# Kernel optimization log

Measured on AMD Instinct MI355X. Metric: run time of the kernel, lower is better.

## Reference

```python
import jax, jax.numpy as jnp
import numpy as np

T = 8192   # sequence length (= max_seq_len)
E = 1024   # embedding dim
D = 11     # hard-coded projection dim in source


def setup_inputs() -> dict:
    key = jax.random.key(0)
    ks = jax.random.split(key, 6)
    s_e = 1.0 / np.sqrt(E)
    s_d = 1.0 / np.sqrt(D)
    return {
        "x": jax.random.randint(ks[0], (T,), 0, 32000, dtype=jnp.int64),
        "x_embeddings": jax.random.normal(ks[1], (T, E), dtype=jnp.float32),
        "Wk": jax.random.normal(ks[2], (D, E), dtype=jnp.float32) * s_e,
        "bk": jnp.zeros((D,), dtype=jnp.float32),
        "Wq": jax.random.normal(ks[3], (D, E), dtype=jnp.float32) * s_e,
        "bq": jnp.zeros((D,), dtype=jnp.float32),
        "Wv": jax.random.normal(ks[4], (D, E), dtype=jnp.float32) * s_e,
        "bv": jnp.zeros((D,), dtype=jnp.float32),
        "Wf": jax.random.normal(ks[5], (E, D), dtype=jnp.float32) * s_d,
        "bf": jnp.zeros((E,), dtype=jnp.float32),
    }


def reference(x, x_embeddings, Wk, bk, Wq, bq, Wv, bv, Wf, bf):
    t = x.shape[0]  # static under jit
    k = x_embeddings @ Wk.T + bk            # [T, D]
    q = x_embeddings @ Wq.T + bq            # [T, D]
    v = x_embeddings @ Wv.T + bv            # [T, D]
    att = q @ k.T                           # [T, T]; NOTE: no 1/sqrt(D) scaling in source
    causal = jnp.tril(jnp.ones((t, t), dtype=bool))
    att = jnp.where(causal, att, -jnp.inf)
    att = jax.nn.softmax(att, axis=1)       # dim=1 as in source
    res = att @ v                           # [T, D]
    return res @ Wf.T + bf                  # [T, E]
```

## Files before the change

### kernel.cpp

```cpp
#include <hip/hip_runtime.h>

#define T_SEQ 8192
#define E_DIM 1024
#define QS 36
#define QNEC 16
#define QKC 64
#define QX4 16
#define QXST 17
#define QRB 64
#define AJC 64
#define ARB 128
#define KVW 24
#define TR 16
#define LOG2E 1.4426950408889634f

__device__ __forceinline__ float2 pkfma(float2 a, float2 b, float2 c) {
    return make_float2(fmaf(a.x, b.x, c.x), fmaf(a.y, b.y, c.y));
}
__device__ __forceinline__ float2 f2(float x, float y) { return make_float2(x, y); }


__global__ __launch_bounds__(256) void prep_wf(const float* __restrict__ Wf,
                                               float* __restrict__ Wfp) {
    int id = blockIdx.x * 256 + threadIdx.x;
    if (id >= E_DIM * 12) return;
    int e = id / 12, d = id % 12;
    Wfp[id] = (d < 11) ? Wf[(size_t)e * 11 + d] : 0.f;
}

__global__ __launch_bounds__(256) void qkv_proj(
    const float* __restrict__ xe,
    const float* __restrict__ Wk, const float* __restrict__ bk,
    const float* __restrict__ Wq, const float* __restrict__ bq,
    const float* __restrict__ Wv, const float* __restrict__ bv,
    float* __restrict__ partQ) {
    const int row0 = blockIdx.x * QRB;
    const int ec = blockIdx.y;
    const int lane = threadIdx.x & 63;
    const int wg = threadIdx.x >> 6;
    const int cb = ec * QKC;

    __shared__ float4 xT[QRB * QXST];
    __shared__ float4 wT[36 * QX4];

#pragma unroll
    for (int t = 0; t < 4; ++t) {
        int idx = threadIdx.x + t * 256;
        int r = idx >> 4, c4 = idx & 15;
        xT[r * QXST + c4] =
            *(const float4*)(xe + (size_t)(row0 + r) * E_DIM + cb + c4 * 4);
    }
    for (int idx = threadIdx.x; idx < 36 * QX4; idx += 256) {
        int r = idx >> 4, c4 = idx & 15;
        float4 v = make_float4(0.f, 0.f, 0.f, 0.f);
        if (r < 33) {
            const float* base = (r < 11) ? (Wk + (size_t)r * E_DIM)
                              : (r < 22) ? (Wq + (size_t)(r - 11) * E_DIM)
                                         : (Wv + (size_t)(r - 22) * E_DIM);
            v = *(const float4*)(base + cb + c4 * 4);
        }
        wT[idx] = v;
    }
    __syncthreads();

    float2 acc[9];
#pragma unroll
    for (int k = 0; k < 9; ++k) acc[k] = f2(0.f, 0.f);

    const float4* xr = xT + lane * QXST;
    const float4* wr = wT + wg * 9 * QX4;
#pragma unroll 4
    for (int c4 = 0; c4 < QX4; ++c4) {
        float4 xv = xr[c4];
#pragma unroll
        for (int k = 0; k < 9; ++k) {
            float4 wv = wr[k * QX4 + c4];
            acc[k] = pkfma(f2(xv.x, xv.y), f2(wv.x, wv.y), acc[k]);
            acc[k] = pkfma(f2(xv.z, xv.w), f2(wv.z, wv.w), acc[k]);
        }
    }

    __syncthreads();
    float* res = (float*)xT;
#pragma unroll
    for (int k = 0; k < 9; ++k) {
        int o = wg * 9 + k;
        bool live = (o < 33);
        int c = (o < 11) ? o : (o < 22) ? o + 1 : (o < 33) ? o + 2
              : (o == 33) ? 11 : (o == 34) ? 23 : 35;
        float b = 0.f;
        if (ec == 0 && live)
            b = (o < 11) ? bk[o] : (o < 22) ? bq[o - 11] : bv[o - 22];
        res[lane * 36 + c] = live ? (acc[k].x + acc[k].y + b) : 0.f;
    }
    __syncthreads();

    float4* dst = (float4*)(partQ + ((size_t)ec * T_SEQ + row0) * QS);
    for (int idx = threadIdx.x; idx < QRB * 9; idx += 256) {
        int r = idx / 9, f = idx % 9;
        dst[idx] = *(const float4*)(res + r * 36 + f * 4);
    }
}

__global__ __launch_bounds__(256) void reduceQ(const float* __restrict__ partQ,
                                               float* __restrict__ qkvF) {
    const size_t idx = (size_t)blockIdx.x * 256 + threadIdx.x;
    const float4* p = (const float4*)partQ;
    const size_t cs = (size_t)T_SEQ * (QS / 4);
    float4 s = make_float4(0.f, 0.f, 0.f, 0.f);
#pragma unroll
    for (int c = 0; c < QNEC; ++c) {
        float4 a = p[idx + (size_t)c * cs];
        s.x += a.x; s.y += a.y; s.z += a.z; s.w += a.w;
    }
    ((float4*)qkvF)[idx] = s;
}

__global__ __launch_bounds__(64) void attn(const float* __restrict__ qkvF,
                                           float* __restrict__ part) {
    const int b = blockIdx.x;
    int rb = 0;
    while ((rb + 1) * (rb + 2) / 2 <= b) ++rb;
    const int s = b - rb * (rb + 1) / 2;
    const int lane = threadIdx.x;
    const int r0 = rb * ARB + lane * 2;

    const float* qp0 = qkvF + (size_t)r0 * QS + 12;
    const float* qp1 = qp0 + QS;
    float2 qa[6], qb[6];
#pragma unroll
    for (int d = 0; d < 5; ++d) {
        qa[d] = f2(qp0[2 * d], qp0[2 * d + 1]);
        qb[d] = f2(qp1[2 * d], qp1[2 * d + 1]);
    }
    qa[5] = f2(qp0[10], 0.f);
    qb[5] = f2(qp1[10], 0.f);

    float2 oa[6], ob[6];
#pragma unroll
    for (int d = 0; d < 6; ++d) { oa[d] = f2(0.f, 0.f); ob[d] = f2(0.f, 0.f); }

    __shared__ float kv[AJC * KVW];

#pragma unroll
    for (int pass = 0; pass < 2; ++pass) {
        const int jc = pass ? (2 * rb + 1 - s) : s;
        const int j0 = jc * AJC;
        if (pass) __syncthreads();
#pragma unroll
        for (int t = 0; t < 6; ++t) {
            int idx = lane + t * 64;
            int row = idx / 6, f = idx % 6;
            int srcOff = f * 4 + (f >= 3 ? 12 : 0);
            float4 v = *(const float4*)(qkvF + (size_t)(j0 + row) * QS + srcOff);
            *(float4*)(kv + row * KVW + f * 4) = v;
        }
        __syncthreads();

        for (int jj = 0; jj < AJC; ++jj) {
            const float* kp = kv + jj * KVW;
            const float4 kA = *(const float4*)(kp);
            const float4 kB = *(const float4*)(kp + 4);
            const float4 kC = *(const float4*)(kp + 8);
            const float4 vA = *(const float4*)(kp + 12);
            const float4 vB = *(const float4*)(kp + 16);
            const float4 vC = *(const float4*)(kp + 20);
            const float2 k01 = f2(kA.x, kA.y), k23 = f2(kA.z, kA.w);
            const float2 k45 = f2(kB.x, kB.y), k67 = f2(kB.z, kB.w);
            const float2 k89 = f2(kC.x, kC.y), kXp = f2(kC.z, kC.w);

            float2 sa = pkfma(qa[0], k01, pkfma(qa[1], k23, pkfma(qa[2], k45,
                        pkfma(qa[3], k67, pkfma(qa[4], k89,
                        pkfma(qa[5], kXp, f2(0.f, 0.f)))))));
            float2 sb = pkfma(qb[0], k01, pkfma(qb[1], k23, pkfma(qb[2], k45,
                        pkfma(qb[3], k67, pkfma(qb[4], k89,
                        pkfma(qb[5], kXp, f2(0.f, 0.f)))))));
            float pa = __expf(sa.x + sa.y);
            float pb = __expf(sb.x + sb.y);
            const int j = j0 + jj;
            pa = (j <= r0)     ? pa : 0.f;
            pb = (j <= r0 + 1) ? pb : 0.f;
            float2 pa2 = f2(pa, pa), pb2 = f2(pb, pb);
            oa[0] = pkfma(pa2, f2(vA.x, vA.y), oa[0]);
            oa[1] = pkfma(pa2, f2(vA.z, vA.w), oa[1]);
            oa[2] = pkfma(pa2, f2(vB.x, vB.y), oa[2]);
            oa[3] = pkfma(pa2, f2(vB.z, vB.w), oa[3]);
            oa[4] = pkfma(pa2, f2(vC.x, vC.y), oa[4]);
            oa[5] = pkfma(pa2, f2(vC.z, 1.f),  oa[5]);
            ob[0] = pkfma(pb2, f2(vA.x, vA.y), ob[0]);
            ob[1] = pkfma(pb2, f2(vA.z, vA.w), ob[1]);
            ob[2] = pkfma(pb2, f2(vB.x, vB.y), ob[2]);
            ob[3] = pkfma(pb2, f2(vB.z, vB.w), ob[3]);
            ob[4] = pkfma(pb2, f2(vC.x, vC.y), ob[4]);
            ob[5] = pkfma(pb2, f2(vC.z, 1.f),  ob[5]);
        }
    }

    float* d0 = part + ((size_t)s * T_SEQ + r0) * 12;
    float4 t;
    t.x = oa[0].x; t.y = oa[0].y; t.z = oa[1].x; t.w = oa[1].y; *(float4*)(d0 + 0) = t;
    t.x = oa[2].x; t.y = oa[2].y; t.z = oa[3].x; t.w = oa[3].y; *(float4*)(d0 + 4) = t;
    t.x = oa[4].x; t.y = oa[4].y; t.z = oa[5].x; t.w = oa[5].y; *(float4*)(d0 + 8) = t;
    float* d1 = d0 + 12;
    t.x = ob[0].x; t.y = ob[0].y; t.z = ob[1].x; t.w = ob[1].y; *(float4*)(d1 + 0) = t;
    t.x = ob[2].x; t.y = ob[2].y; t.z = ob[3].x; t.w = ob[3].y; *(float4*)(d1 + 4) = t;
    t.x = ob[4].x; t.y = ob[4].y; t.z = ob[5].x; t.w = ob[5].y; *(float4*)(d1 + 8) = t;
}

__global__ __launch_bounds__(256) void pass2(const float* __restrict__ part,
                                             const float* __restrict__ Wfp,
                                             const float* __restrict__ bf,
                                             float* __restrict__ out) {
    const int t0 = blockIdx.x * TR;
    __shared__ float res[TR][12];
    const int cnt = t0 / ARB + 1;
    if (threadIdx.x < TR * 12) {
        const float* p = part + (size_t)t0 * 12 + threadIdx.x;
        const size_t S = (size_t)T_SEQ * 12;
        float v[4];
#pragma unroll
        for (int u = 0; u < 4; ++u) v[u] = 0.f;
        int c = 0;
        for (; c + 4 <= cnt; c += 4) {
#pragma unroll
            for (int u = 0; u < 4; ++u) v[u] += p[(size_t)(c + u) * S];
        }
        for (; c < cnt; ++c) v[0] += p[(size_t)c * S];
        float sum = (v[0] + v[1]) + (v[2] + v[3]);
        const int d = threadIdx.x % 12;
        res[threadIdx.x / 12][d] = (d == 11) ? (1.f / sum) : sum;
    }
    __syncthreads();

    const int e0 = threadIdx.x * 4;
    float4 wf[4][3];
#pragma unroll
    for (int ee = 0; ee < 4; ++ee) {
        const float4* wp = (const float4*)(Wfp + (size_t)(e0 + ee) * 12);
        wf[ee][0] = wp[0]; wf[ee][1] = wp[1]; wf[ee][2] = wp[2];
    }
    const float4 bv = *(const float4*)(bf + e0);

    for (int r = 0; r < TR; ++r) {
        float rr[12];
#pragma unroll
        for (int d = 0; d < 12; ++d) rr[d] = res[r][d];
        float2 a0 = f2(0.f, 0.f), a1 = a0, a2 = a0, a3 = a0;
#pragma unroll
        for (int d = 0; d < 10; d += 2) {
            float2 rv = f2(rr[d], rr[d + 1]);
            a0 = pkfma(rv, f2(((const float*)&wf[0][0])[d], ((const float*)&wf[0][0])[d + 1]), a0);
            a1 = pkfma(rv, f2(((const float*)&wf[1][0])[d], ((const float*)&wf[1][0])[d + 1]), a1);
            a2 = pkfma(rv, f2(((const float*)&wf[2][0])[d], ((const float*)&wf[2][0])[d + 1]), a2);
            a3 = pkfma(rv, f2(((const float*)&wf[3][0])[d], ((const float*)&wf[3][0])[d + 1]), a3);
        }
        const float rl = rr[11];
        float4 ov;
        ov.x = (a0.x + a0.y + rr[10] * wf[0][2].z) * rl + bv.x;
        ov.y = (a1.x + a1.y + rr[10] * wf[1][2].z) * rl + bv.y;
        ov.z = (a2.x + a2.y + rr[10] * wf[2][2].z) * rl + bv.z;
        ov.w = (a3.x + a3.y + rr[10] * wf[3][2].z) * rl + bv.w;
        *(float4*)(out + (size_t)(t0 + r) * E_DIM + e0) = ov;
    }
}

extern "C" void kernel_launch(void* const* d_in, const int* in_sizes, int n_in,
                              void* d_out, int out_size, void* d_ws, size_t ws_size,
                              hipStream_t stream) {
    const float* xe = (const float*)d_in[1];
    const float* Wk = (const float*)d_in[2];
    const float* bk = (const float*)d_in[3];
    const float* Wq = (const float*)d_in[4];
    const float* bq = (const float*)d_in[5];
    const float* Wv = (const float*)d_in[6];
    const float* bv = (const float*)d_in[7];
    const float* Wf = (const float*)d_in[8];
    const float* bf = (const float*)d_in[9];
    float* out = (float*)d_out;

    float* qkvF  = (float*)d_ws;
    float* wfp   = qkvF + (size_t)T_SEQ * QS;
    float* partQ = wfp + (size_t)E_DIM * 12;
    float* part  = partQ;

    prep_wf<<<(E_DIM * 12 + 255) / 256, 256, 0, stream>>>(Wf, wfp);
    qkv_proj<<<dim3(T_SEQ / QRB, QNEC), 256, 0, stream>>>(xe, Wk, bk, Wq, bq, Wv, bv, partQ);
    reduceQ<<<(T_SEQ * (QS / 4)) / 256, 256, 0, stream>>>(partQ, qkvF);
    const int nrb = T_SEQ / ARB;
    attn<<<nrb * (nrb + 1) / 2, 64, 0, stream>>>(qkvF, part);
    pass2<<<T_SEQ / TR, 256, 0, stream>>>(part, wfp, bf, out);
}
```

Before: 177.8 us.

## Split attention into single-chunk blocks and reduce partials with atomics

Each attention block now handles a single 64-key chunk instead of two paired chunks, which doubles the grid. Partial outputs are accumulated straight into one zero-initialised buffer with float atomicAdd, so the strided multi-partial reduction in pass2 goes away. The zeroing is folded into the existing prep kernel. This trades a longer reduction read and an extra partial buffer for atomic contention (up to 128 adds per element) and non-deterministic summation order.

```diff
diff --git a/kernel.cpp b/kernel.cpp
--- a/kernel.cpp
+++ b/kernel.cpp
@@ -12,7 +12,6 @@
 #define ARB 128
 #define KVW 24
 #define TR 16
-#define LOG2E 1.4426950408889634f
 
 __device__ __forceinline__ float2 pkfma(float2 a, float2 b, float2 c) {
     return make_float2(fmaf(a.x, b.x, c.x), fmaf(a.y, b.y, c.y));
@@ -20,12 +19,17 @@
 __device__ __forceinline__ float2 f2(float x, float y) { return make_float2(x, y); }
 
 
-__global__ __launch_bounds__(256) void prep_wf(const float* __restrict__ Wf,
-                                               float* __restrict__ Wfp) {
+__global__ __launch_bounds__(256) void prep(const float* __restrict__ Wf,
+                                            float* __restrict__ Wfp,
+                                            float* __restrict__ part1) {
     int id = blockIdx.x * 256 + threadIdx.x;
-    if (id >= E_DIM * 12) return;
-    int e = id / 12, d = id % 12;
-    Wfp[id] = (d < 11) ? Wf[(size_t)e * 11 + d] : 0.f;
+    if (id < E_DIM * 12) {
+        int e = id / 12, d = id % 12;
+        Wfp[id] = (d < 11) ? Wf[(size_t)e * 11 + d] : 0.f;
+    } else {
+        int j = id - E_DIM * 12;
+        if (j < T_SEQ * 12) part1[j] = 0.f;
+    }
 }
 
 __global__ __launch_bounds__(256) void qkv_proj(
@@ -117,13 +121,14 @@
 }
 
 __global__ __launch_bounds__(64) void attn(const float* __restrict__ qkvF,
-                                           float* __restrict__ part) {
+                                           float* __restrict__ part1) {
     const int b = blockIdx.x;
     int rb = 0;
-    while ((rb + 1) * (rb + 2) / 2 <= b) ++rb;
-    const int s = b - rb * (rb + 1) / 2;
+    while ((rb + 1) * (rb + 2) <= b) ++rb;
+    const int jc = b - rb * (rb + 1);
     const int lane = threadIdx.x;
     const int r0 = rb * ARB + lane * 2;
+    const int j0 = jc * AJC;
 
     const float* qp0 = qkvF + (size_t)r0 * QS + 12;
     const float* qp1 = qp0 + QS;
@@ -143,92 +148,79 @@
     __shared__ float kv[AJC * KVW];
 
 #pragma unroll
-    for (int pass = 0; pass < 2; ++pass) {
-        const int jc = pass ? (2 * rb + 1 - s) : s;
-        const int j0 = jc * AJC;
-        if (pass) __syncthreads();
-#pragma unroll
-        for (int t = 0; t < 6; ++t) {
-            int idx = lane + t * 64;
-            int row = idx / 6, f = idx % 6;
-            int srcOff = f * 4 + (f >= 3 ? 12 : 0);
-            float4 v = *(const float4*)(qkvF + (size_t)(j0 + row) * QS + srcOff);
-            *(float4*)(kv + row * KVW + f * 4) = v;
-        }
-        __syncthreads();
-
-        for (int jj = 0; jj < AJC; ++jj) {
-            const float* kp = kv + jj * KVW;
-            const float4 kA = *(const float4*)(kp);
-            const float4 kB = *(const float4*)(kp + 4);
-            const float4 kC = *(const float4*)(kp + 8);
-            const float4 vA = *(const float4*)(kp + 12);
-            const float4 vB = *(const float4*)(kp + 16);
-            const float4 vC = *(const float4*)(kp + 20);
-            const float2 k01 = f2(kA.x, kA.y), k23 = f2(kA.z, kA.w);
-            const float2 k45 = f2(kB.x, kB.y), k67 = f2(kB.z, kB.w);
-            const float2 k89 = f2(kC.x, kC.y), kXp = f2(kC.z, kC.w);
-
-            float2 sa = pkfma(qa[0], k01, pkfma(qa[1], k23, pkfma(qa[2], k45,
-                        pkfma(qa[3], k67, pkfma(qa[4], k89,
-                        pkfma(qa[5], kXp, f2(0.f, 0.f)))))));
-            float2 sb = pkfma(qb[0], k01, pkfma(qb[1], k23, pkfma(qb[2], k45,
-                        pkfma(qb[3], k67, pkfma(qb[4], k89,
-                        pkfma(qb[5], kXp, f2(0.f, 0.f)))))));
-            float pa = __expf(sa.x + sa.y);
-            float pb = __expf(sb.x + sb.y);
-            const int j = j0 + jj;
-            pa = (j <= r0)     ? pa : 0.f;
-            pb = (j <= r0 + 1) ? pb : 0.f;
-            float2 pa2 = f2(pa, pa), pb2 = f2(pb, pb);
-            oa[0] = pkfma(pa2, f2(vA.x, vA.y), oa[0]);
-            oa[1] = pkfma(pa2, f2(vA.z, vA.w), oa[1]);
-            oa[2] = pkfma(pa2, f2(vB.x, vB.y), oa[2]);
-            oa[3] = pkfma(pa2, f2(vB.z, vB.w), oa[3]);
-            oa[4] = pkfma(pa2, f2(vC.x, vC.y), oa[4]);
-            oa[5] = pkfma(pa2, f2(vC.z, 1.f),  oa[5]);
-            ob[0] = pkfma(pb2, f2(vA.x, vA.y), ob[0]);
-            ob[1] = pkfma(pb2, f2(vA.z, vA.w), ob[1]);
-            ob[2] = pkfma(pb2, f2(vB.x, vB.y), ob[2]);
-            ob[3] = pkfma(pb2, f2(vB.z, vB.w), ob[3]);
-            ob[4] = pkfma(pb2, f2(vC.x, vC.y), ob[4]);
-            ob[5] = pkfma(pb2, f2(vC.z, 1.f),  ob[5]);
-        }
-    }
-
-    float* d0 = part + ((size_t)s * T_SEQ + r0) * 12;
-    float4 t;
-    t.x = oa[0].x; t.y = oa[0].y; t.z = oa[1].x; t.w = oa[1].y; *(float4*)(d0 + 0) = t;
-    t.x = oa[2].x; t.y = oa[2].y; t.z = oa[3].x; t.w = oa[3].y; *(float4*)(d0 + 4) = t;
-    t.x = oa[4].x; t.y = oa[4].y; t.z = oa[5].x; t.w = oa[5].y; *(float4*)(d0 + 8) = t;
+    for (int t = 0; t < 6; ++t) {
+        int idx = lane + t * 64;
+        int row = idx / 6, f = idx % 6;
+        int srcOff = f * 4 + (f >= 3 ? 12 : 0);
+        float4 v = *(const float4*)(qkvF + (size_t)(j0 + row) * QS + srcOff);
+        *(float4*)(kv + row * KVW + f * 4) = v;
+    }
+    __syncthreads();
+
+    for (int jj = 0; jj < AJC; ++jj) {
+        const float* kp = kv + jj * KVW;
+        const float4 kA = *(const float4*)(kp);
+        const float4 kB = *(const float4*)(kp + 4);
+        const float4 kC = *(const float4*)(kp + 8);
+        const float4 vA = *(const float4*)(kp + 12);
+        const float4 vB = *(const float4*)(kp + 16);
+        const float4 vC = *(const float4*)(kp + 20);
+        const float2 k01 = f2(kA.x, kA.y), k23 = f2(kA.z, kA.w);
+        const float2 k45 = f2(kB.x, kB.y), k67 = f2(kB.z, kB.w);
+        const float2 k89 = f2(kC.x, kC.y), kXp = f2(kC.z, kC.w);
+
+        float2 sa = pkfma(qa[0], k01, pkfma(qa[1], k23, pkfma(qa[2], k45,
+                    pkfma(qa[3], k67, pkfma(qa[4], k89,
+                    pkfma(qa[5], kXp, f2(0.f, 0.f)))))));
+        float2 sb = pkfma(qb[0], k01, pkfma(qb[1], k23, pkfma(qb[2], k45,
+                    pkfma(qb[3], k67, pkfma(qb[4], k89,
+                    pkfma(qb[5], kXp, f2(0.f, 0.f)))))));
+        float pa = __expf(sa.x + sa.y);
+        float pb = __expf(sb.x + sb.y);
+        const int j = j0 + jj;
+        pa = (j <= r0)     ? pa : 0.f;
+        pb = (j <= r0 + 1) ? pb : 0.f;
+        float2 pa2 = f2(pa, pa), pb2 = f2(pb, pb);
+        oa[0] = pkfma(pa2, f2(vA.x, vA.y), oa[0]);
+        oa[1] = pkfma(pa2, f2(vA.z, vA.w), oa[1]);
+        oa[2] = pkfma(pa2, f2(vB.x, vB.y), oa[2]);
+        oa[3] = pkfma(pa2, f2(vB.z, vB.w), oa[3]);
+        oa[4] = pkfma(pa2, f2(vC.x, vC.y), oa[4]);
+        oa[5] = pkfma(pa2, f2(vC.z, 1.f),  oa[5]);
+        ob[0] = pkfma(pb2, f2(vA.x, vA.y), ob[0]);
+        ob[1] = pkfma(pb2, f2(vA.z, vA.w), ob[1]);
+        ob[2] = pkfma(pb2, f2(vB.x, vB.y), ob[2]);
+        ob[3] = pkfma(pb2, f2(vB.z, vB.w), ob[3]);
+        ob[4] = pkfma(pb2, f2(vC.x, vC.y), ob[4]);
+        ob[5] = pkfma(pb2, f2(vC.z, 1.f),  ob[5]);
+    }
+
+    float* d0 = part1 + (size_t)r0 * 12;
+    atomicAdd(d0 + 0,  oa[0].x); atomicAdd(d0 + 1,  oa[0].y);
+    atomicAdd(d0 + 2,  oa[1].x); atomicAdd(d0 + 3,  oa[1].y);
+    atomicAdd(d0 + 4,  oa[2].x); atomicAdd(d0 + 5,  oa[2].y);
+    atomicAdd(d0 + 6,  oa[3].x); atomicAdd(d0 + 7,  oa[3].y);
+    atomicAdd(d0 + 8,  oa[4].x); atomicAdd(d0 + 9,  oa[4].y);
+    atomicAdd(d0 + 10, oa[5].x); atomicAdd(d0 + 11, oa[5].y);
     float* d1 = d0 + 12;
-    t.x = ob[0].x; t.y = ob[0].y; t.z = ob[1].x; t.w = ob[1].y; *(float4*)(d1 + 0) = t;
-    t.x = ob[2].x; t.y = ob[2].y; t.z = ob[3].x; t.w = ob[3].y; *(float4*)(d1 + 4) = t;
-    t.x = ob[4].x; t.y = ob[4].y; t.z = ob[5].x; t.w = ob[5].y; *(float4*)(d1 + 8) = t;
-}
-
-__global__ __launch_bounds__(256) void pass2(const float* __restrict__ part,
+    atomicAdd(d1 + 0,  ob[0].x); atomicAdd(d1 + 1,  ob[0].y);
+    atomicAdd(d1 + 2,  ob[1].x); atomicAdd(d1 + 3,  ob[1].y);
+    atomicAdd(d1 + 4,  ob[2].x); atomicAdd(d1 + 5,  ob[2].y);
+    atomicAdd(d1 + 6,  ob[3].x); atomicAdd(d1 + 7,  ob[3].y);
+    atomicAdd(d1 + 8,  ob[4].x); atomicAdd(d1 + 9,  ob[4].y);
+    atomicAdd(d1 + 10, ob[5].x); atomicAdd(d1 + 11, ob[5].y);
+}
+
+__global__ __launch_bounds__(256) void pass2(const float* __restrict__ part1,
                                              const float* __restrict__ Wfp,
                                              const float* __restrict__ bf,
                                              float* __restrict__ out) {
     const int t0 = blockIdx.x * TR;
     __shared__ float res[TR][12];
-    const int cnt = t0 / ARB + 1;
     if (threadIdx.x < TR * 12) {
-        const float* p = part + (size_t)t0 * 12 + threadIdx.x;
-        const size_t S = (size_t)T_SEQ * 12;
-        float v[4];
-#pragma unroll
-        for (int u = 0; u < 4; ++u) v[u] = 0.f;
-        int c = 0;
-        for (; c + 4 <= cnt; c += 4) {
-#pragma unroll
-            for (int u = 0; u < 4; ++u) v[u] += p[(size_t)(c + u) * S];
-        }
-        for (; c < cnt; ++c) v[0] += p[(size_t)c * S];
-        float sum = (v[0] + v[1]) + (v[2] + v[3]);
+        float v = part1[(size_t)t0 * 12 + threadIdx.x];
         const int d = threadIdx.x % 12;
-        res[threadIdx.x / 12][d] = (d == 11) ? (1.f / sum) : sum;
+        res[threadIdx.x / 12][d] = (d == 11) ? (1.f / v) : v;
     }
     __syncthreads();
 
@@ -281,12 +273,12 @@
     float* qkvF  = (float*)d_ws;
     float* wfp   = qkvF + (size_t)T_SEQ * QS;
     float* partQ = wfp + (size_t)E_DIM * 12;
-    float* part  = partQ;
-
-    prep_wf<<<(E_DIM * 12 + 255) / 256, 256, 0, stream>>>(Wf, wfp);
+    float* part1 = partQ + (size_t)QNEC * T_SEQ * QS;
+
+    prep<<<(E_DIM * 12 + T_SEQ * 12 + 255) / 256, 256, 0, stream>>>(Wf, wfp, part1);
     qkv_proj<<<dim3(T_SEQ / QRB, QNEC), 256, 0, stream>>>(xe, Wk, bk, Wq, bq, Wv, bv, partQ);
     reduceQ<<<(T_SEQ * (QS / 4)) / 256, 256, 0, stream>>>(partQ, qkvF);
     const int nrb = T_SEQ / ARB;
-    attn<<<nrb * (nrb + 1) / 2, 64, 0, stream>>>(qkvF, part);
-    pass2<<<T_SEQ / TR, 256, 0, stream>>>(part, wfp, bf, out);
-}
+    attn<<<nrb * (nrb + 1), 64, 0, stream>>>(qkvF, part1);
+    pass2<<<T_SEQ / TR, 256, 0, stream>>>(part1, wfp, bf, out);
+}
```

Measured after the change: 531.2 us. +198.7%, slower.

## Split attention key chunks across two waves and drop Wf prep kernel

Applied to the files above, without the earlier changes.

The attention kernel now runs 128 threads per block, and each wave handles one of two adjacent 64-key chunks in parallel instead of one wave looping over two paired chunks. Partials are indexed by key chunk, so pass2 sums twice as many partial slices (2*rb+2). The separate Wf padding kernel is removed and pass2 reads the unpadded Wf directly with scalar loads. This trades one kernel launch and serial per-wave work for more partial-sum traffic in pass2 and a different causal load balance, since the earlier pairing of chunks s and 2rb+1-s gave every block equal work.

```diff
diff --git a/kernel.cpp b/kernel.cpp
--- a/kernel.cpp
+++ b/kernel.cpp
@@ -11,22 +11,14 @@
 #define AJC 64
 #define ARB 128
 #define KVW 24
+#define NSLOT 128
 #define TR 16
-#define LOG2E 1.4426950408889634f
 
 __device__ __forceinline__ float2 pkfma(float2 a, float2 b, float2 c) {
     return make_float2(fmaf(a.x, b.x, c.x), fmaf(a.y, b.y, c.y));
 }
 __device__ __forceinline__ float2 f2(float x, float y) { return make_float2(x, y); }
 
-
-__global__ __launch_bounds__(256) void prep_wf(const float* __restrict__ Wf,
-                                               float* __restrict__ Wfp) {
-    int id = blockIdx.x * 256 + threadIdx.x;
-    if (id >= E_DIM * 12) return;
-    int e = id / 12, d = id % 12;
-    Wfp[id] = (d < 11) ? Wf[(size_t)e * 11 + d] : 0.f;
-}
 
 __global__ __launch_bounds__(256) void qkv_proj(
     const float* __restrict__ xe,
@@ -116,14 +108,17 @@
     ((float4*)qkvF)[idx] = s;
 }
 
-__global__ __launch_bounds__(64) void attn(const float* __restrict__ qkvF,
-                                           float* __restrict__ part) {
+__global__ __launch_bounds__(128) void attn(const float* __restrict__ qkvF,
+                                            float* __restrict__ part) {
     const int b = blockIdx.x;
     int rb = 0;
     while ((rb + 1) * (rb + 2) / 2 <= b) ++rb;
-    const int s = b - rb * (rb + 1) / 2;
-    const int lane = threadIdx.x;
+    const int p = b - rb * (rb + 1) / 2;
+    const int lane = threadIdx.x & 63;
+    const int wid = threadIdx.x >> 6;
+    const int jc = 2 * p + wid;
     const int r0 = rb * ARB + lane * 2;
+    const int j0 = jc * AJC;
 
     const float* qp0 = qkvF + (size_t)r0 * QS + 12;
     const float* qp1 = qp0 + QS;
@@ -140,63 +135,58 @@
 #pragma unroll
     for (int d = 0; d < 6; ++d) { oa[d] = f2(0.f, 0.f); ob[d] = f2(0.f, 0.f); }
 
-    __shared__ float kv[AJC * KVW];
-
-#pragma unroll
-    for (int pass = 0; pass < 2; ++pass) {
-        const int jc = pass ? (2 * rb + 1 - s) : s;
-        const int j0 = jc * AJC;
-        if (pass) __syncthreads();
-#pragma unroll
-        for (int t = 0; t < 6; ++t) {
-            int idx = lane + t * 64;
-            int row = idx / 6, f = idx % 6;
-            int srcOff = f * 4 + (f >= 3 ? 12 : 0);
-            float4 v = *(const float4*)(qkvF + (size_t)(j0 + row) * QS + srcOff);
-            *(float4*)(kv + row * KVW + f * 4) = v;
-        }
-        __syncthreads();
-
-        for (int jj = 0; jj < AJC; ++jj) {
-            const float* kp = kv + jj * KVW;
-            const float4 kA = *(const float4*)(kp);
-            const float4 kB = *(const float4*)(kp + 4);
-            const float4 kC = *(const float4*)(kp + 8);
-            const float4 vA = *(const float4*)(kp + 12);
-            const float4 vB = *(const float4*)(kp + 16);
-            const float4 vC = *(const float4*)(kp + 20);
-            const float2 k01 = f2(kA.x, kA.y), k23 = f2(kA.z, kA.w);
-            const float2 k45 = f2(kB.x, kB.y), k67 = f2(kB.z, kB.w);
-            const float2 k89 = f2(kC.x, kC.y), kXp = f2(kC.z, kC.w);
-
-            float2 sa = pkfma(qa[0], k01, pkfma(qa[1], k23, pkfma(qa[2], k45,
-                        pkfma(qa[3], k67, pkfma(qa[4], k89,
-                        pkfma(qa[5], kXp, f2(0.f, 0.f)))))));
-            float2 sb = pkfma(qb[0], k01, pkfma(qb[1], k23, pkfma(qb[2], k45,
-                        pkfma(qb[3], k67, pkfma(qb[4], k89,
-                        pkfma(qb[5], kXp, f2(0.f, 0.f)))))));
-            float pa = __expf(sa.x + sa.y);
-            float pb = __expf(sb.x + sb.y);
-            const int j = j0 + jj;
-            pa = (j <= r0)     ? pa : 0.f;
-            pb = (j <= r0 + 1) ? pb : 0.f;
-            float2 pa2 = f2(pa, pa), pb2 = f2(pb, pb);
-            oa[0] = pkfma(pa2, f2(vA.x, vA.y), oa[0]);
-            oa[1] = pkfma(pa2, f2(vA.z, vA.w), oa[1]);
-            oa[2] = pkfma(pa2, f2(vB.x, vB.y), oa[2]);
-            oa[3] = pkfma(pa2, f2(vB.z, vB.w), oa[3]);
-            oa[4] = pkfma(pa2, f2(vC.x, vC.y), oa[4]);
-            oa[5] = pkfma(pa2, f2(vC.z, 1.f),  oa[5]);
-            ob[0] = pkfma(pb2, f2(vA.x, vA.y), ob[0]);
-            ob[1] = pkfma(pb2, f2(vA.z, vA.w), ob[1]);
-            ob[2] = pkfma(pb2, f2(vB.x, vB.y), ob[2]);
-            ob[3] = pkfma(pb2, f2(vB.z, vB.w), ob[3]);
-            ob[4] = pkfma(pb2, f2(vC.x, vC.y), ob[4]);
-            ob[5] = pkfma(pb2, f2(vC.z, 1.f),  ob[5]);
-        }
-    }
-
-    float* d0 = part + ((size_t)s * T_SEQ + r0) * 12;
+    __shared__ float kvs[2][AJC * KVW];
+    float* kv = kvs[wid];
+
+#pragma unroll
+    for (int t = 0; t < 6; ++t) {
+        int idx = lane + t * 64;
+        int row = idx / 6, f = idx % 6;
+        int srcOff = f * 4 + (f >= 3 ? 12 : 0);
+        float4 v = *(const float4*)(qkvF + (size_t)(j0 + row) * QS + srcOff);
+        *(float4*)(kv + row * KVW + f * 4) = v;
+    }
+    __syncthreads();
+
+    for (int jj = 0; jj < AJC; ++jj) {
+        const float* kp = kv + jj * KVW;
+        const float4 kA = *(const float4*)(kp);
+        const float4 kB = *(const float4*)(kp + 4);
+        const float4 kC = *(const float4*)(kp + 8);
+        const float4 vA = *(const float4*)(kp + 12);
+        const float4 vB = *(const float4*)(kp + 16);
+        const float4 vC = *(const float4*)(kp + 20);
+        const float2 k01 = f2(kA.x, kA.y), k23 = f2(kA.z, kA.w);
+        const float2 k45 = f2(kB.x, kB.y), k67 = f2(kB.z, kB.w);
+        const float2 k89 = f2(kC.x, kC.y), kXp = f2(kC.z, kC.w);
+
+        float2 sa = pkfma(qa[0], k01, pkfma(qa[1], k23, pkfma(qa[2], k45,
+                    pkfma(qa[3], k67, pkfma(qa[4], k89,
+                    pkfma(qa[5], kXp, f2(0.f, 0.f)))))));
+        float2 sb = pkfma(qb[0], k01, pkfma(qb[1], k23, pkfma(qb[2], k45,
+                    pkfma(qb[3], k67, pkfma(qb[4], k89,
+                    pkfma(qb[5], kXp, f2(0.f, 0.f)))))));
+        float pa = __expf(sa.x + sa.y);
+        float pb = __expf(sb.x + sb.y);
+        const int j = j0 + jj;
+        pa = (j <= r0)     ? pa : 0.f;
+        pb = (j <= r0 + 1) ? pb : 0.f;
+        float2 pa2 = f2(pa, pa), pb2 = f2(pb, pb);
+        oa[0] = pkfma(pa2, f2(vA.x, vA.y), oa[0]);
+        oa[1] = pkfma(pa2, f2(vA.z, vA.w), oa[1]);
+        oa[2] = pkfma(pa2, f2(vB.x, vB.y), oa[2]);
+        oa[3] = pkfma(pa2, f2(vB.z, vB.w), oa[3]);
+        oa[4] = pkfma(pa2, f2(vC.x, vC.y), oa[4]);
+        oa[5] = pkfma(pa2, f2(vC.z, 1.f),  oa[5]);
+        ob[0] = pkfma(pb2, f2(vA.x, vA.y), ob[0]);
+        ob[1] = pkfma(pb2, f2(vA.z, vA.w), ob[1]);
+        ob[2] = pkfma(pb2, f2(vB.x, vB.y), ob[2]);
+        ob[3] = pkfma(pb2, f2(vB.z, vB.w), ob[3]);
+        ob[4] = pkfma(pb2, f2(vC.x, vC.y), ob[4]);
+        ob[5] = pkfma(pb2, f2(vC.z, 1.f),  ob[5]);
+    }
+
+    float* d0 = part + ((size_t)jc * T_SEQ + r0) * 12;
     float4 t;
     t.x = oa[0].x; t.y = oa[0].y; t.z = oa[1].x; t.w = oa[1].y; *(float4*)(d0 + 0) = t;
     t.x = oa[2].x; t.y = oa[2].y; t.z = oa[3].x; t.w = oa[3].y; *(float4*)(d0 + 4) = t;
@@ -208,12 +198,12 @@
 }
 
 __global__ __launch_bounds__(256) void pass2(const float* __restrict__ part,
-                                             const float* __restrict__ Wfp,
+                                             const float* __restrict__ Wf,
                                              const float* __restrict__ bf,
                                              float* __restrict__ out) {
     const int t0 = blockIdx.x * TR;
     __shared__ float res[TR][12];
-    const int cnt = t0 / ARB + 1;
+    const int cnt = 2 * (t0 / ARB) + 2;
     if (threadIdx.x < TR * 12) {
         const float* p = part + (size_t)t0 * 12 + threadIdx.x;
         const size_t S = (size_t)T_SEQ * 12;
@@ -233,12 +223,12 @@
     __syncthreads();
 
     const int e0 = threadIdx.x * 4;
-    float4 wf[4][3];
-#pragma unroll
-    for (int ee = 0; ee < 4; ++ee) {
-        const float4* wp = (const float4*)(Wfp + (size_t)(e0 + ee) * 12);
-        wf[ee][0] = wp[0]; wf[ee][1] = wp[1]; wf[ee][2] = wp[2];
-    }
+    float w[4][11];
+    const float* wp = Wf + (size_t)e0 * 11;
+#pragma unroll
+    for (int ee = 0; ee < 4; ++ee)
+#pragma unroll
+        for (int i = 0; i < 11; ++i) w[ee][i] = wp[ee * 11 + i];
     const float4 bv = *(const float4*)(bf + e0);
 
     for (int r = 0; r < TR; ++r) {
@@ -249,17 +239,17 @@
 #pragma unroll
         for (int d = 0; d < 10; d += 2) {
             float2 rv = f2(rr[d], rr[d + 1]);
-            a0 = pkfma(rv, f2(((const float*)&wf[0][0])[d], ((const float*)&wf[0][0])[d + 1]), a0);
-            a1 = pkfma(rv, f2(((const float*)&wf[1][0])[d], ((const float*)&wf[1][0])[d + 1]), a1);
-            a2 = pkfma(rv, f2(((const float*)&wf[2][0])[d], ((const float*)&wf[2][0])[d + 1]), a2);
-            a3 = pkfma(rv, f2(((const float*)&wf[3][0])[d], ((const float*)&wf[3][0])[d + 1]), a3);
+            a0 = pkfma(rv, f2(w[0][d], w[0][d + 1]), a0);
+            a1 = pkfma(rv, f2(w[1][d], w[1][d + 1]), a1);
+            a2 = pkfma(rv, f2(w[2][d], w[2][d + 1]), a2);
+            a3 = pkfma(rv, f2(w[3][d], w[3][d + 1]), a3);
         }
         const float rl = rr[11];
         float4 ov;
-        ov.x = (a0.x + a0.y + rr[10] * wf[0][2].z) * rl + bv.x;
-        ov.y = (a1.x + a1.y + rr[10] * wf[1][2].z) * rl + bv.y;
-        ov.z = (a2.x + a2.y + rr[10] * wf[2][2].z) * rl + bv.z;
-        ov.w = (a3.x + a3.y + rr[10] * wf[3][2].z) * rl + bv.w;
+        ov.x = (a0.x + a0.y + rr[10] * w[0][10]) * rl + bv.x;
+        ov.y = (a1.x + a1.y + rr[10] * w[1][10]) * rl + bv.y;
+        ov.z = (a2.x + a2.y + rr[10] * w[2][10]) * rl + bv.z;
+        ov.w = (a3.x + a3.y + rr[10] * w[3][10]) * rl + bv.w;
         *(float4*)(out + (size_t)(t0 + r) * E_DIM + e0) = ov;
     }
 }
@@ -279,14 +269,12 @@
     float* out = (float*)d_out;
 
     float* qkvF  = (float*)d_ws;
-    float* wfp   = qkvF + (size_t)T_SEQ * QS;
-    float* partQ = wfp + (size_t)E_DIM * 12;
+    float* partQ = qkvF + (size_t)T_SEQ * QS;
     float* part  = partQ;
 
-    prep_wf<<<(E_DIM * 12 + 255) / 256, 256, 0, stream>>>(Wf, wfp);
     qkv_proj<<<dim3(T_SEQ / QRB, QNEC), 256, 0, stream>>>(xe, Wk, bk, Wq, bq, Wv, bv, partQ);
     reduceQ<<<(T_SEQ * (QS / 4)) / 256, 256, 0, stream>>>(partQ, qkvF);
     const int nrb = T_SEQ / ARB;
-    attn<<<nrb * (nrb + 1) / 2, 64, 0, stream>>>(qkvF, part);
-    pass2<<<T_SEQ / TR, 256, 0, stream>>>(part, wfp, bf, out);
-}
+    attn<<<nrb * (nrb + 1) / 2, 128, 0, stream>>>(qkvF, part);
+    pass2<<<T_SEQ / TR, 256, 0, stream>>>(part, Wf, bf, out);
+}
```

Result: no change. 176.6 us (-0.7%).
